# Optimization experiments

Hardware: AMD Instinct MI355X
Metric: run time of the kernel (lower is better)

The kernel has to match this reference:

```python
import jax, jax.numpy as jnp
import numpy as np

B, T, I, H, C = 4096, 512, 1, 32, 2


def setup_inputs() -> dict:
    key = jax.random.key(0)
    ks = jax.random.split(key, 7)
    k_ih = 1.0 / np.sqrt(H)  # PyTorch GRU init bound (uniform, but normal*scale is fine for a numeric reference)
    x = jax.random.normal(ks[0], (B, T, I), dtype=jnp.float32)
    W_ih = jax.random.normal(ks[1], (3 * H, I), dtype=jnp.float32) * k_ih
    W_hh = jax.random.normal(ks[2], (3 * H, H), dtype=jnp.float32) * k_ih
    b_ih = jax.random.normal(ks[3], (3 * H,), dtype=jnp.float32) * k_ih
    b_hh = jax.random.normal(ks[4], (3 * H,), dtype=jnp.float32) * k_ih
    fc_w = jax.random.normal(ks[5], (C, H), dtype=jnp.float32) * k_ih
    fc_b = jax.random.normal(ks[6], (C,), dtype=jnp.float32) * k_ih
    return {"x": x, "W_ih": W_ih, "W_hh": W_hh, "b_ih": b_ih, "b_hh": b_hh, "fc_w": fc_w, "fc_b": fc_b}


def _gru_last_hidden(x, W_ih, W_hh, b_ih, b_hh):
    # Precompute input projections for all timesteps: [B, T, 3H]
    xg = jnp.einsum('bti,gi->btg', x, W_ih) + b_ih
    xg_t = jnp.swapaxes(xg, 0, 1)  # [T, B, 3H] for scan over time
    h0 = jnp.zeros((x.shape[0], W_hh.shape[1]), dtype=x.dtype)

    def step(h, xg_step):
        hg = h @ W_hh.T + b_hh  # [B, 3H]
        xr, xz, xn = jnp.split(xg_step, 3, axis=-1)
        hr, hz, hn = jnp.split(hg, 3, axis=-1)
        r = jax.nn.sigmoid(xr + hr)
        z = jax.nn.sigmoid(xz + hz)
        n = jnp.tanh(xn + r * hn)
        h_new = (1.0 - z) * n + z * h  # PyTorch GRU update rule
        return h_new, None

    hT, _ = jax.lax.scan(step, h0, xg_t)
    return hT  # [B, H] == out[:, -1, :]


def reference(x, W_ih, W_hh, b_ih, b_hh, fc_w, fc_b):
    hT = _gru_last_hidden(x, W_ih, W_hh, b_ih, b_hh)
    return hT @ fc_w.T + fc_b  # [B, C]
```

## Files before the change

### kernel.cpp

```cpp
#include <hip/hip_runtime.h>
#include <hip/hip_bf16.h>


__device__ __forceinline__ float sigm(float a) {
    float e = __builtin_amdgcn_exp2f(a * -1.442695041f);
    return __builtin_amdgcn_rcpf(1.0f + e);
}

__global__ __launch_bounds__(256, 2)
void gru_fused_kernel(const float* __restrict__ x,
                      const float* __restrict__ W_ih,
                      const float* __restrict__ W_hh,
                      const float* __restrict__ b_ih,
                      const float* __restrict__ b_hh,
                      const float* __restrict__ fc_w,
                      const float* __restrict__ fc_b,
                      float* __restrict__ out)
{
    const int tid = threadIdx.x;
    const int j   = tid & 31;
    const int g   = tid >> 5;
    const int bb  = blockIdx.x * 8 + g;

    __shared__ float xs[8 * 516];
    __shared__ int h8[8][8];

    {
        const float* xbase = x + (size_t)blockIdx.x * 8 * 512;
        #pragma unroll
        for (int k = 0; k < 16; ++k) {
            int idx = tid + k * 256;
            int b   = idx >> 9, p = idx & 511;
            xs[b * 516 + p] = xbase[idx];
        }
    }

    int qr0,qr1,qr2,qr3,qr4,qr5,qr6,qr7;
    int qz0,qz1,qz2,qz3,qz4,qz5,qz6,qz7;
    int qn0,qn1,qn2,qn3,qn4,qn5,qn6,qn7;
    float srj, szj, snj;
    {
#define AMAX4(v) am = fmaxf(am, fmaxf(fmaxf(fabsf(v.x), fabsf(v.y)), \
                                      fmaxf(fabsf(v.z), fabsf(v.w))));
#define PACKQ(dst, v) dst = (((int)__builtin_rintf((v).x * qs) & 0xff)       ) | \
                            (((int)__builtin_rintf((v).y * qs) & 0xff) <<  8) | \
                            (((int)__builtin_rintf((v).z * qs) & 0xff) << 16) | \
                            (((int)__builtin_rintf((v).w * qs) & 0xff) << 24);
#define QROW(base, q0,q1,q2,q3,q4,q5,q6,q7, scale)                              \
        {                                                                       \
            const float4* p = reinterpret_cast<const float4*>(base);            \
            float4 v0=p[0],v1=p[1],v2=p[2],v3=p[3],v4=p[4],v5=p[5],v6=p[6],v7=p[7]; \
            float am = 1e-20f;                                                  \
            AMAX4(v0) AMAX4(v1) AMAX4(v2) AMAX4(v3)                             \
            AMAX4(v4) AMAX4(v5) AMAX4(v6) AMAX4(v7)                             \
            float qs = 127.0f / am;                                             \
            scale = am * (1.0f / 16129.0f);                                     \
            PACKQ(q0, v0) PACKQ(q1, v1) PACKQ(q2, v2) PACKQ(q3, v3)             \
            PACKQ(q4, v4) PACKQ(q5, v5) PACKQ(q6, v6) PACKQ(q7, v7)             \
        }
        QROW(W_hh + j * 32,        qr0,qr1,qr2,qr3,qr4,qr5,qr6,qr7, srj)
        QROW(W_hh + (32 + j) * 32, qz0,qz1,qz2,qz3,qz4,qz5,qz6,qz7, szj)
        QROW(W_hh + (64 + j) * 32, qn0,qn1,qn2,qn3,qn4,qn5,qn6,qn7, snj)
#undef QROW
#undef AMAX4
#undef PACKQ
    }

    const float br   = b_ih[j]      + b_hh[j];
    const float bz   = b_ih[32 + j] + b_hh[32 + j];
    const float bin  = b_ih[64 + j];
    const float bhn  = b_hh[64 + j];
    const float wihr = W_ih[j];
    const float wihz = W_ih[32 + j];
    const float wihn = W_ih[64 + j];

    float h = 0.0f;
    if (j < 8) h8[g][j] = 0;
    __syncthreads();

    const float* xc = &xs[g * 516];

    #pragma unroll 8
    for (int t = 0; t < 512; ++t) {
        float xb = xc[t];

        const int4* q8 = reinterpret_cast<const int4*>(&h8[g][0]);
        int4 Qa = q8[0], Qb = q8[1];

        int iar = 0, iaz = 0, ian = 0;
        iar = __builtin_amdgcn_sdot4(qr0, Qa.x, iar, false);
        iaz = __builtin_amdgcn_sdot4(qz0, Qa.x, iaz, false);
        ian = __builtin_amdgcn_sdot4(qn0, Qa.x, ian, false);
        iar = __builtin_amdgcn_sdot4(qr1, Qa.y, iar, false);
        iaz = __builtin_amdgcn_sdot4(qz1, Qa.y, iaz, false);
        ian = __builtin_amdgcn_sdot4(qn1, Qa.y, ian, false);
        iar = __builtin_amdgcn_sdot4(qr2, Qa.z, iar, false);
        iaz = __builtin_amdgcn_sdot4(qz2, Qa.z, iaz, false);
        ian = __builtin_amdgcn_sdot4(qn2, Qa.z, ian, false);
        iar = __builtin_amdgcn_sdot4(qr3, Qa.w, iar, false);
        iaz = __builtin_amdgcn_sdot4(qz3, Qa.w, iaz, false);
        ian = __builtin_amdgcn_sdot4(qn3, Qa.w, ian, false);
        iar = __builtin_amdgcn_sdot4(qr4, Qb.x, iar, false);
        iaz = __builtin_amdgcn_sdot4(qz4, Qb.x, iaz, false);
        ian = __builtin_amdgcn_sdot4(qn4, Qb.x, ian, false);
        iar = __builtin_amdgcn_sdot4(qr5, Qb.y, iar, false);
        iaz = __builtin_amdgcn_sdot4(qz5, Qb.y, iaz, false);
        ian = __builtin_amdgcn_sdot4(qn5, Qb.y, ian, false);
        iar = __builtin_amdgcn_sdot4(qr6, Qb.z, iar, false);
        iaz = __builtin_amdgcn_sdot4(qz6, Qb.z, iaz, false);
        ian = __builtin_amdgcn_sdot4(qn6, Qb.z, ian, false);
        iar = __builtin_amdgcn_sdot4(qr7, Qb.w, iar, false);
        iaz = __builtin_amdgcn_sdot4(qz7, Qb.w, iaz, false);
        ian = __builtin_amdgcn_sdot4(qn7, Qb.w, ian, false);

        float ar = fmaf((float)iar, srj, fmaf(xb, wihr, br));
        float az = fmaf((float)iaz, szj, fmaf(xb, wihz, bz));
        float an = fmaf((float)ian, snj, bhn);

        float r = sigm(ar);
        float z = sigm(az);
        float npre = fmaf(r, an, fmaf(xb, wihn, bin));
        float e2 = __builtin_amdgcn_exp2f(npre * 2.885390082f);
        float t2 = __builtin_amdgcn_rcpf(1.0f + e2);
        float n  = fmaf(-2.0f, t2, 1.0f);
        h = fmaf(z, h - n, n);

        int qh = (int)__builtin_rintf(h * 127.0f);
        reinterpret_cast<unsigned char*>(&h8[g][0])[j] = (unsigned char)qh;
    }

    float s0 = h * fc_w[j];
    float s1 = h * fc_w[32 + j];
    #pragma unroll
    for (int off = 16; off >= 1; off >>= 1) {
        s0 += __shfl_xor(s0, off, 32);
        s1 += __shfl_xor(s1, off, 32);
    }
    if (j == 0) {
        out[(size_t)bb * 2 + 0] = s0 + fc_b[0];
        out[(size_t)bb * 2 + 1] = s1 + fc_b[1];
    }
}

extern "C" void kernel_launch(void* const* d_in, const int* in_sizes, int n_in,
                              void* d_out, int out_size, void* d_ws, size_t ws_size,
                              hipStream_t stream)
{
    const float* x    = (const float*)d_in[0];
    const float* W_ih = (const float*)d_in[1];
    const float* W_hh = (const float*)d_in[2];
    const float* b_ih = (const float*)d_in[3];
    const float* b_hh = (const float*)d_in[4];
    const float* fc_w = (const float*)d_in[5];
    const float* fc_b = (const float*)d_in[6];
    float* out = (float*)d_out;

    dim3 grid(512), block(256);
    hipLaunchKernelGGL(gru_fused_kernel, grid, block, 0, stream,
                       x, W_ih, W_hh, b_ih, b_hh, fc_w, fc_b, out);
}
```

Baseline: 135.7 us.

## Process two batch sequences per 32-lane group to raise ILP in GRU recurrence

```diff
diff --git a/kernel.cpp b/kernel.cpp
--- a/kernel.cpp
+++ b/kernel.cpp
@@ -7,7 +7,7 @@
     return __builtin_amdgcn_rcpf(1.0f + e);
 }
 
-__global__ __launch_bounds__(256, 2)
+__global__ __launch_bounds__(256, 1)
 void gru_fused_kernel(const float* __restrict__ x,
                       const float* __restrict__ W_ih,
                       const float* __restrict__ W_hh,
@@ -20,15 +20,15 @@
     const int tid = threadIdx.x;
     const int j   = tid & 31;
     const int g   = tid >> 5;
-    const int bb  = blockIdx.x * 8 + g;
+    const int lb0 = 2 * g, lb1 = 2 * g + 1;
 
-    __shared__ float xs[8 * 516];
-    __shared__ int h8[8][8];
+    __shared__ float xs[16 * 516];
+    __shared__ int h8[16][8];
 
     {
-        const float* xbase = x + (size_t)blockIdx.x * 8 * 512;
+        const float* xbase = x + (size_t)blockIdx.x * 16 * 512;
         #pragma unroll
-        for (int k = 0; k < 16; ++k) {
+        for (int k = 0; k < 32; ++k) {
             int idx = tid + k * 256;
             int b   = idx >> 9, p = idx & 511;
             xs[b * 516 + p] = xbase[idx];
@@ -74,71 +74,97 @@
     const float wihz = W_ih[32 + j];
     const float wihn = W_ih[64 + j];
 
-    float h = 0.0f;
-    if (j < 8) h8[g][j] = 0;
+    float h0 = 0.0f, h1 = 0.0f;
+    if (j < 8) { h8[lb0][j] = 0; h8[lb1][j] = 0; }
     __syncthreads();
 
-    const float* xc = &xs[g * 516];
+    const float* xc0 = &xs[lb0 * 516];
+    const float* xc1 = &xs[lb1 * 516];
 
-    #pragma unroll 8
+    #pragma unroll 4
     for (int t = 0; t < 512; ++t) {
-        float xb = xc[t];
+        float xb0 = xc0[t];
+        float xb1 = xc1[t];
 
-        const int4* q8 = reinterpret_cast<const int4*>(&h8[g][0]);
-        int4 Qa = q8[0], Qb = q8[1];
+        const int4* q80 = reinterpret_cast<const int4*>(&h8[lb0][0]);
+        const int4* q81 = reinterpret_cast<const int4*>(&h8[lb1][0]);
+        int4 Qa0 = q80[0], Qb0 = q80[1];
+        int4 Qa1 = q81[0], Qb1 = q81[1];
 
-        int iar = 0, iaz = 0, ian = 0;
-        iar = __builtin_amdgcn_sdot4(qr0, Qa.x, iar, false);
-        iaz = __builtin_amdgcn_sdot4(qz0, Qa.x, iaz, false);
-        ian = __builtin_amdgcn_sdot4(qn0, Qa.x, ian, false);
-        iar = __builtin_amdgcn_sdot4(qr1, Qa.y, iar, false);
-        iaz = __builtin_amdgcn_sdot4(qz1, Qa.y, iaz, false);
-        ian = __builtin_amdgcn_sdot4(qn1, Qa.y, ian, false);
-        iar = __builtin_amdgcn_sdot4(qr2, Qa.z, iar, false);
-        iaz = __builtin_amdgcn_sdot4(qz2, Qa.z, iaz, false);
-        ian = __builtin_amdgcn_sdot4(qn2, Qa.z, ian, false);
-        iar = __builtin_amdgcn_sdot4(qr3, Qa.w, iar, false);
-        iaz = __builtin_amdgcn_sdot4(qz3, Qa.w, iaz, false);
-        ian = __builtin_amdgcn_sdot4(qn3, Qa.w, ian, false);
-        iar = __builtin_amdgcn_sdot4(qr4, Qb.x, iar, false);
-        iaz = __builtin_amdgcn_sdot4(qz4, Qb.x, iaz, false);
-        ian = __builtin_amdgcn_sdot4(qn4, Qb.x, ian, false);
-        iar = __builtin_amdgcn_sdot4(qr5, Qb.y, iar, false);
-        iaz = __builtin_amdgcn_sdot4(qz5, Qb.y, iaz, false);
-        ian = __builtin_amdgcn_sdot4(qn5, Qb.y, ian, false);
-        iar = __builtin_amdgcn_sdot4(qr6, Qb.z, iar, false);
-        iaz = __builtin_amdgcn_sdot4(qz6, Qb.z, iaz, false);
-        ian = __builtin_amdgcn_sdot4(qn6, Qb.z, ian, false);
-        iar = __builtin_amdgcn_sdot4(qr7, Qb.w, iar, false);
-        iaz = __builtin_amdgcn_sdot4(qz7, Qb.w, iaz, false);
-        ian = __builtin_amdgcn_sdot4(qn7, Qb.w, ian, false);
+        int iar0 = 0, iaz0 = 0, ian0 = 0;
+        int iar1 = 0, iaz1 = 0, ian1 = 0;
+#define SD(QW, HK0, HK1, A0, A1)                                 \
+        A0 = __builtin_amdgcn_sdot4(QW, HK0, A0, false);         \
+        A1 = __builtin_amdgcn_sdot4(QW, HK1, A1, false);
+        SD(qr0, Qa0.x, Qa1.x, iar0, iar1)
+        SD(qz0, Qa0.x, Qa1.x, iaz0, iaz1)
+        SD(qn0, Qa0.x, Qa1.x, ian0, ian1)
+        SD(qr1, Qa0.y, Qa1.y, iar0, iar1)
+        SD(qz1, Qa0.y, Qa1.y, iaz0, iaz1)
+        SD(qn1, Qa0.y, Qa1.y, ian0, ian1)
+        SD(qr2, Qa0.z, Qa1.z, iar0, iar1)
+        SD(qz2, Qa0.z, Qa1.z, iaz0, iaz1)
+        SD(qn2, Qa0.z, Qa1.z, ian0, ian1)
+        SD(qr3, Qa0.w, Qa1.w, iar0, iar1)
+        SD(qz3, Qa0.w, Qa1.w, iaz0, iaz1)
+        SD(qn3, Qa0.w, Qa1.w, ian0, ian1)
+        SD(qr4, Qb0.x, Qb1.x, iar0, iar1)
+        SD(qz4, Qb0.x, Qb1.x, iaz0, iaz1)
+        SD(qn4, Qb0.x, Qb1.x, ian0, ian1)
+        SD(qr5, Qb0.y, Qb1.y, iar0, iar1)
+        SD(qz5, Qb0.y, Qb1.y, iaz0, iaz1)
+        SD(qn5, Qb0.y, Qb1.y, ian0, ian1)
+        SD(qr6, Qb0.z, Qb1.z, iar0, iar1)
+        SD(qz6, Qb0.z, Qb1.z, iaz0, iaz1)
+        SD(qn6, Qb0.z, Qb1.z, ian0, ian1)
+        SD(qr7, Qb0.w, Qb1.w, iar0, iar1)
+        SD(qz7, Qb0.w, Qb1.w, iaz0, iaz1)
+        SD(qn7, Qb0.w, Qb1.w, ian0, ian1)
+#undef SD
 
-        float ar = fmaf((float)iar, srj, fmaf(xb, wihr, br));
-        float az = fmaf((float)iaz, szj, fmaf(xb, wihz, bz));
-        float an = fmaf((float)ian, snj, bhn);
+        float ar0 = fmaf((float)iar0, srj, fmaf(xb0, wihr, br));
+        float ar1 = fmaf((float)iar1, srj, fmaf(xb1, wihr, br));
+        float az0 = fmaf((float)iaz0, szj, fmaf(xb0, wihz, bz));
+        float az1 = fmaf((float)iaz1, szj, fmaf(xb1, wihz, bz));
+        float an0 = fmaf((float)ian0, snj, bhn);
+        float an1 = fmaf((float)ian1, snj, bhn);
 
-        float r = sigm(ar);
-        float z = sigm(az);
-        float npre = fmaf(r, an, fmaf(xb, wihn, bin));
-        float e2 = __builtin_amdgcn_exp2f(npre * 2.885390082f);
-        float t2 = __builtin_amdgcn_rcpf(1.0f + e2);
-        float n  = fmaf(-2.0f, t2, 1.0f);
-        h = fmaf(z, h - n, n);
+        float r0 = sigm(ar0), r1 = sigm(ar1);
+        float z0 = sigm(az0), z1 = sigm(az1);
+        float np0 = fmaf(r0, an0, fmaf(xb0, wihn, bin));
+        float np1 = fmaf(r1, an1, fmaf(xb1, wihn, bin));
+        float e0 = __builtin_amdgcn_exp2f(np0 * 2.885390082f);
+        float e1 = __builtin_amdgcn_exp2f(np1 * 2.885390082f);
+        float t0 = __builtin_amdgcn_rcpf(1.0f + e0);
+        float t1 = __builtin_amdgcn_rcpf(1.0f + e1);
+        float n0 = fmaf(-2.0f, t0, 1.0f);
+        float n1 = fmaf(-2.0f, t1, 1.0f);
+        h0 = fmaf(z0, h0 - n0, n0);
+        h1 = fmaf(z1, h1 - n1, n1);
 
-        int qh = (int)__builtin_rintf(h * 127.0f);
-        reinterpret_cast<unsigned char*>(&h8[g][0])[j] = (unsigned char)qh;
+        int qh0 = (int)__builtin_rintf(h0 * 127.0f);
+        int qh1 = (int)__builtin_rintf(h1 * 127.0f);
+        reinterpret_cast<unsigned char*>(&h8[lb0][0])[j] = (unsigned char)qh0;
+        reinterpret_cast<unsigned char*>(&h8[lb1][0])[j] = (unsigned char)qh1;
     }
 
-    float s0 = h * fc_w[j];
-    float s1 = h * fc_w[32 + j];
+    const float f0 = fc_w[j], f1 = fc_w[32 + j];
+    float s00 = h0 * f0, s01 = h0 * f1;
+    float s10 = h1 * f0, s11 = h1 * f1;
     #pragma unroll
     for (int off = 16; off >= 1; off >>= 1) {
-        s0 += __shfl_xor(s0, off, 32);
-        s1 += __shfl_xor(s1, off, 32);
+        s00 += __shfl_xor(s00, off, 32);
+        s01 += __shfl_xor(s01, off, 32);
+        s10 += __shfl_xor(s10, off, 32);
+        s11 += __shfl_xor(s11, off, 32);
     }
     if (j == 0) {
-        out[(size_t)bb * 2 + 0] = s0 + fc_b[0];
-        out[(size_t)bb * 2 + 1] = s1 + fc_b[1];
+        const size_t gb0 = (size_t)blockIdx.x * 16 + lb0;
+        const size_t gb1 = (size_t)blockIdx.x * 16 + lb1;
+        out[gb0 * 2 + 0] = s00 + fc_b[0];
+        out[gb0 * 2 + 1] = s01 + fc_b[1];
+        out[gb1 * 2 + 0] = s10 + fc_b[0];
+        out[gb1 * 2 + 1] = s11 + fc_b[1];
     }
 }
 
@@ -155,7 +181,7 @@
     const float* fc_b = (const float*)d_in[6];
     float* out = (float*)d_out;
 
-    dim3 grid(512), block(256);
+    dim3 grid(256), block(256);
     hipLaunchKernelGGL(gru_fused_kernel, grid, block, 0, stream,
                        x, W_ih, W_hh, b_ih, b_hh, fc_w, fc_b, out);
 }
```

Result: no change. 137.2 us (+1.1%).

## Exchange quantized hidden state via DPP and ds_swizzle instead of shared memory

Applied to the files above, without the earlier changes.

```diff
diff --git a/kernel.cpp b/kernel.cpp
--- a/kernel.cpp
+++ b/kernel.cpp
@@ -23,7 +23,6 @@
     const int bb  = blockIdx.x * 8 + g;
 
     __shared__ float xs[8 * 516];
-    __shared__ int h8[8][8];
 
     {
         const float* xbase = x + (size_t)blockIdx.x * 8 * 512;
@@ -74,8 +73,11 @@
     const float wihz = W_ih[32 + j];
     const float wihn = W_ih[64 + j];
 
+    const int shamt = (j & 3) * 8;
+
     float h = 0.0f;
-    if (j < 8) h8[g][j] = 0;
+    int hh0 = 0, hh1 = 0, hh2 = 0, hh3 = 0;
+    int hh4 = 0, hh5 = 0, hh6 = 0, hh7 = 0;
     __syncthreads();
 
     const float* xc = &xs[g * 516];
@@ -84,38 +86,36 @@
     for (int t = 0; t < 512; ++t) {
         float xb = xc[t];
 
-        const int4* q8 = reinterpret_cast<const int4*>(&h8[g][0]);
-        int4 Qa = q8[0], Qb = q8[1];
+        int iarA = 0, iazA = 0, ianA = 0;
+        int iarB = 0, iazB = 0, ianB = 0;
+        iarA = __builtin_amdgcn_sdot4(qr0, hh0, iarA, false);
+        iazA = __builtin_amdgcn_sdot4(qz0, hh0, iazA, false);
+        ianA = __builtin_amdgcn_sdot4(qn0, hh0, ianA, false);
+        iarA = __builtin_amdgcn_sdot4(qr1, hh1, iarA, false);
+        iazA = __builtin_amdgcn_sdot4(qz1, hh1, iazA, false);
+        ianA = __builtin_amdgcn_sdot4(qn1, hh1, ianA, false);
+        iarA = __builtin_amdgcn_sdot4(qr2, hh2, iarA, false);
+        iazA = __builtin_amdgcn_sdot4(qz2, hh2, iazA, false);
+        ianA = __builtin_amdgcn_sdot4(qn2, hh2, ianA, false);
+        iarA = __builtin_amdgcn_sdot4(qr3, hh3, iarA, false);
+        iazA = __builtin_amdgcn_sdot4(qz3, hh3, iazA, false);
+        ianA = __builtin_amdgcn_sdot4(qn3, hh3, ianA, false);
+        iarB = __builtin_amdgcn_sdot4(qr4, hh4, iarB, false);
+        iazB = __builtin_amdgcn_sdot4(qz4, hh4, iazB, false);
+        ianB = __builtin_amdgcn_sdot4(qn4, hh4, ianB, false);
+        iarB = __builtin_amdgcn_sdot4(qr5, hh5, iarB, false);
+        iazB = __builtin_amdgcn_sdot4(qz5, hh5, iazB, false);
+        ianB = __builtin_amdgcn_sdot4(qn5, hh5, ianB, false);
+        iarB = __builtin_amdgcn_sdot4(qr6, hh6, iarB, false);
+        iazB = __builtin_amdgcn_sdot4(qz6, hh6, iazB, false);
+        ianB = __builtin_amdgcn_sdot4(qn6, hh6, ianB, false);
+        iarB = __builtin_amdgcn_sdot4(qr7, hh7, iarB, false);
+        iazB = __builtin_amdgcn_sdot4(qz7, hh7, iazB, false);
+        ianB = __builtin_amdgcn_sdot4(qn7, hh7, ianB, false);
 
-        int iar = 0, iaz = 0, ian = 0;
-        iar = __builtin_amdgcn_sdot4(qr0, Qa.x, iar, false);
-        iaz = __builtin_amdgcn_sdot4(qz0, Qa.x, iaz, false);
-        ian = __builtin_amdgcn_sdot4(qn0, Qa.x, ian, false);
-        iar = __builtin_amdgcn_sdot4(qr1, Qa.y, iar, false);
-        iaz = __builtin_amdgcn_sdot4(qz1, Qa.y, iaz, false);
-        ian = __builtin_amdgcn_sdot4(qn1, Qa.y, ian, false);
-        iar = __builtin_amdgcn_sdot4(qr2, Qa.z, iar, false);
-        iaz = __builtin_amdgcn_sdot4(qz2, Qa.z, iaz, false);
-        ian = __builtin_amdgcn_sdot4(qn2, Qa.z, ian, false);
-        iar = __builtin_amdgcn_sdot4(qr3, Qa.w, iar, false);
-        iaz = __builtin_amdgcn_sdot4(qz3, Qa.w, iaz, false);
-        ian = __builtin_amdgcn_sdot4(qn3, Qa.w, ian, false);
-        iar = __builtin_amdgcn_sdot4(qr4, Qb.x, iar, false);
-        iaz = __builtin_amdgcn_sdot4(qz4, Qb.x, iaz, false);
-        ian = __builtin_amdgcn_sdot4(qn4, Qb.x, ian, false);
-        iar = __builtin_amdgcn_sdot4(qr5, Qb.y, iar, false);
-        iaz = __builtin_amdgcn_sdot4(qz5, Qb.y, iaz, false);
-        ian = __builtin_amdgcn_sdot4(qn5, Qb.y, ian, false);
-        iar = __builtin_amdgcn_sdot4(qr6, Qb.z, iar, false);
-        iaz = __builtin_amdgcn_sdot4(qz6, Qb.z, iaz, false);
-        ian = __builtin_amdgcn_sdot4(qn6, Qb.z, ian, false);
-        iar = __builtin_amdgcn_sdot4(qr7, Qb.w, iar, false);
-        iaz = __builtin_amdgcn_sdot4(qz7, Qb.w, iaz, false);
-        ian = __builtin_amdgcn_sdot4(qn7, Qb.w, ian, false);
-
-        float ar = fmaf((float)iar, srj, fmaf(xb, wihr, br));
-        float az = fmaf((float)iaz, szj, fmaf(xb, wihz, bz));
-        float an = fmaf((float)ian, snj, bhn);
+        float ar = fmaf((float)(iarA + iarB), srj, fmaf(xb, wihr, br));
+        float az = fmaf((float)(iazA + iazB), szj, fmaf(xb, wihz, bz));
+        float an = fmaf((float)(ianA + ianB), snj, bhn);
 
         float r = sigm(ar);
         float z = sigm(az);
@@ -125,8 +125,19 @@
         float n  = fmaf(-2.0f, t2, 1.0f);
         h = fmaf(z, h - n, n);
 
-        int qh = (int)__builtin_rintf(h * 127.0f);
-        reinterpret_cast<unsigned char*>(&h8[g][0])[j] = (unsigned char)qh;
+        int qh = ((int)__builtin_rintf(h * 127.0f) & 0xff) << shamt;
+        int d1 = __builtin_amdgcn_update_dpp(0, qh, 0xB1, 0xF, 0xF, true);
+        int o1 = qh | d1;
+        int d2 = __builtin_amdgcn_update_dpp(0, o1, 0x4E, 0xF, 0xF, true);
+        int w  = o1 | d2;
+        hh0 = __builtin_amdgcn_ds_swizzle(w, (0  << 5));
+        hh1 = __builtin_amdgcn_ds_swizzle(w, (4  << 5));
+        hh2 = __builtin_amdgcn_ds_swizzle(w, (8  << 5));
+        hh3 = __builtin_amdgcn_ds_swizzle(w, (12 << 5));
+        hh4 = __builtin_amdgcn_ds_swizzle(w, (16 << 5));
+        hh5 = __builtin_amdgcn_ds_swizzle(w, (20 << 5));
+        hh6 = __builtin_amdgcn_ds_swizzle(w, (24 << 5));
+        hh7 = __builtin_amdgcn_ds_swizzle(w, (28 << 5));
     }
 
     float s0 = h * fc_w[j];
```

Result: slower. 155.6 us (+14.7%).
